# Optimization experiments

Measured on AMD Instinct MI355X. Metric: run time of the kernel, lower is better.

The kernel has to match this reference:

```python
import jax, jax.numpy as jnp
import numpy as np

N_NODES = 50000
N_EDGES = 800000
HIDDEN = 64
NUM_FEATURES = 1
OUT_DIM = 2


def setup_inputs() -> dict:
    key = jax.random.key(0)
    k = jax.random.split(key, 6)
    x = jax.random.normal(k[0], (N_NODES, NUM_FEATURES), dtype=jnp.float32)
    edge_index = jax.random.randint(k[1], (2, N_EDGES), 0, N_NODES, dtype=jnp.int32)
    # GCNConv params (PyG default: glorot weight, zero bias; random here for testing)
    W1 = jax.random.normal(k[2], (NUM_FEATURES, HIDDEN), dtype=jnp.float32) * 0.5
    b1 = jax.random.normal(k[3], (HIDDEN,), dtype=jnp.float32) * 0.1
    W2 = jax.random.normal(k[4], (HIDDEN, OUT_DIM), dtype=jnp.float32) * 0.1
    b2 = jax.random.normal(k[5], (OUT_DIM,), dtype=jnp.float32) * 0.1
    return {"x": x, "edge_index": edge_index, "W1": W1, "b1": b1, "W2": W2, "b2": b2}


def _gcn_norm(edge_index, num_nodes):
    # PyG gcn_norm with add_self_loops=True, symmetric normalization
    row, col = edge_index[0], edge_index[1]
    loop = jnp.arange(num_nodes, dtype=row.dtype)
    row = jnp.concatenate([row, loop])
    col = jnp.concatenate([col, loop])
    ew = jnp.ones(row.shape[0], dtype=jnp.float32)
    deg = jax.ops.segment_sum(ew, col, num_segments=num_nodes)  # in-degree incl. self-loop
    dinv = jnp.where(deg > 0, jax.lax.rsqrt(deg), 0.0)
    norm = dinv[row] * dinv[col]  # [E+N]
    return row, col, norm


def _gcn_conv(x, row, col, norm, W, b, num_nodes):
    h = x @ W                                  # [N, out] transform first (out <= in here is fine)
    msg = h[row] * norm[:, None]               # gather + scale, [E+N, out]
    out = jax.ops.segment_sum(msg, col, num_segments=num_nodes)  # scatter-add at targets
    return out + b


def reference(x, edge_index, W1, b1, W2, b2):
    row, col, norm = _gcn_norm(edge_index, N_NODES)
    h = _gcn_conv(x, row, col, norm, W1, b1, N_NODES)
    h = jax.nn.relu(h)
    out = _gcn_conv(h, row, col, norm, W2, b2, N_NODES)
    return out
```

## Files before the change

kernel.cpp:

```cpp
#include <hip/hip_runtime.h>
#include <math.h>

#define N_NODES 50000
#define N_EDGES 800000
#define HIDDEN  64
#define MAXDEG  64


__global__ void k_build(const int* __restrict__ row, const int* __restrict__ col,
                        int* __restrict__ cnt, unsigned short* __restrict__ ell) {
    int e = blockIdx.x * blockDim.x + threadIdx.x;
    if (e < N_EDGES) {
        int c = col[e];
        int rk = atomicAdd(&cnt[c], 1);
        if (rk < MAXDEG) ell[rk * N_NODES + c] = (unsigned short)row[e];
    }
}

__global__ void k_dinvg(const int* __restrict__ cnt, const float* __restrict__ x,
                        float* __restrict__ dinv, float* __restrict__ g) {
    int i = blockIdx.x * blockDim.x + threadIdx.x;
    if (i < N_NODES) {
        float di = rsqrtf((float)(cnt[i] + 1));
        dinv[i] = di;
        g[i] = di * x[i];
    }
}

__global__ void k_layer1(const unsigned short* __restrict__ ell,
                         const int* __restrict__ cnt, const float* __restrict__ g,
                         const float* __restrict__ dinv,
                         const float* __restrict__ W1, const float* __restrict__ b1,
                         const float* __restrict__ W2, float2* __restrict__ z) {
    int n = blockIdx.x * blockDim.x + threadIdx.x;
    if (n >= N_NODES) return;
    int d = cnt[n]; if (d > MAXDEG) d = MAXDEG;
    float acc = 0.0f;
    int j = 0;
    for (; j + 2 <= d; j += 2) {
        int r0 = ell[j * N_NODES + n];
        int r1 = ell[(j + 1) * N_NODES + n];
        acc += g[r0] + g[r1];
    }
    if (j < d) acc += g[ell[j * N_NODES + n]];
    float di = dinv[n];
    float sv = di * (acc + g[n]);
    float y0 = 0.0f, y1 = 0.0f;
#pragma unroll
    for (int k = 0; k < HIDDEN; ++k) {
        float h = fmaxf(sv * W1[k] + b1[k], 0.0f);
        y0 += h * W2[2 * k];
        y1 += h * W2[2 * k + 1];
    }
    z[n] = make_float2(di * y0, di * y1);
}

__global__ void k_layer2(const unsigned short* __restrict__ ell,
                         const int* __restrict__ cnt, const float2* __restrict__ z,
                         const float* __restrict__ dinv, const float* __restrict__ b2,
                         float* __restrict__ out) {
    int n = blockIdx.x * blockDim.x + threadIdx.x;
    if (n >= N_NODES) return;
    int d = cnt[n]; if (d > MAXDEG) d = MAXDEG;
    float T0 = 0.0f, T1 = 0.0f;
    int j = 0;
    for (; j + 2 <= d; j += 2) {
        int r0 = ell[j * N_NODES + n];
        int r1 = ell[(j + 1) * N_NODES + n];
        float2 v0 = z[r0], v1 = z[r1];
        T0 += v0.x + v1.x;
        T1 += v0.y + v1.y;
    }
    if (j < d) {
        float2 v = z[ell[j * N_NODES + n]];
        T0 += v.x; T1 += v.y;
    }
    float di = dinv[n];
    float2 zn = z[n];
    out[2 * n]     = di * (T0 + zn.x) + b2[0];
    out[2 * n + 1] = di * (T1 + zn.y) + b2[1];
}


extern "C" void kernel_launch(void* const* d_in, const int* in_sizes, int n_in,
                              void* d_out, int out_size, void* d_ws, size_t ws_size,
                              hipStream_t stream) {
    const float* x  = (const float*)d_in[0];
    const int*   ei = (const int*)d_in[1];
    const float* W1 = (const float*)d_in[2];
    const float* b1 = (const float*)d_in[3];
    const float* W2 = (const float*)d_in[4];
    const float* b2 = (const float*)d_in[5];
    float* out = (float*)d_out;

    const int* row = ei;
    const int* col = ei + N_EDGES;

    int*    ws   = (int*)d_ws;
    int*    cnt  = ws;
    float*  dinv = (float*)(ws + 1 * N_NODES);
    float*  g    = (float*)(ws + 2 * N_NODES);
    float2* z    = (float2*)(ws + 3 * N_NODES);
    unsigned short* ell = (unsigned short*)(ws + 5 * N_NODES);

    const int BE = 256, BN = 128;
    const int gE = (N_EDGES + BE - 1) / BE;
    const int gN = (N_NODES + BN - 1) / BN;

    hipMemsetAsync(cnt, 0, N_NODES * sizeof(int), stream);
    k_build<<<gE, BE, 0, stream>>>(row, col, cnt, ell);
    k_dinvg<<<gN, BN, 0, stream>>>(cnt, x, dinv, g);
    k_layer1<<<gN, BN, 0, stream>>>(ell, cnt, g, dinv, W1, b1, W2, z);
    k_layer2<<<gN, BN, 0, stream>>>(ell, cnt, z, dinv, b2, out);
}
```

Baseline: 127.8 us.

## Fuse degree-normalization into layer kernels and vectorize edge build

Removes the separate dinv/g kernel: layer1 now recomputes rsqrt(deg+1)*x for each gathered neighbor, and both layers compute their own dinv from the count. The build kernel handles two edges per thread with int2 loads, block size goes from 128 to 256 with launch bounds, and the output is written as float2. This saves one launch and the dinv/g buffers, but layer1 now does two random gathers (cnt and x) per neighbor instead of one.

Measured after the change: 128.3 us. Within noise of the previous version (+0.4%).

```diff
diff --git a/kernel.cpp b/kernel.cpp
--- a/kernel.cpp
+++ b/kernel.cpp
@@ -7,31 +7,30 @@
 #define MAXDEG  64
 
 
-__global__ void k_build(const int* __restrict__ row, const int* __restrict__ col,
-                        int* __restrict__ cnt, unsigned short* __restrict__ ell) {
-    int e = blockIdx.x * blockDim.x + threadIdx.x;
-    if (e < N_EDGES) {
+__global__ __launch_bounds__(256)
+void k_build(const int* __restrict__ row, const int* __restrict__ col,
+             int* __restrict__ cnt, unsigned short* __restrict__ ell) {
+    int i = blockIdx.x * blockDim.x + threadIdx.x;
+    int e = i * 2;
+    if (e + 1 < N_EDGES) {
+        int2 c2 = *(const int2*)(col + e);
+        int2 r2 = *(const int2*)(row + e);
+        int rk0 = atomicAdd(&cnt[c2.x], 1);
+        int rk1 = atomicAdd(&cnt[c2.y], 1);
+        if (rk0 < MAXDEG) ell[rk0 * N_NODES + c2.x] = (unsigned short)r2.x;
+        if (rk1 < MAXDEG) ell[rk1 * N_NODES + c2.y] = (unsigned short)r2.y;
+    } else if (e < N_EDGES) {
         int c = col[e];
         int rk = atomicAdd(&cnt[c], 1);
         if (rk < MAXDEG) ell[rk * N_NODES + c] = (unsigned short)row[e];
     }
 }
 
-__global__ void k_dinvg(const int* __restrict__ cnt, const float* __restrict__ x,
-                        float* __restrict__ dinv, float* __restrict__ g) {
-    int i = blockIdx.x * blockDim.x + threadIdx.x;
-    if (i < N_NODES) {
-        float di = rsqrtf((float)(cnt[i] + 1));
-        dinv[i] = di;
-        g[i] = di * x[i];
-    }
-}
-
-__global__ void k_layer1(const unsigned short* __restrict__ ell,
-                         const int* __restrict__ cnt, const float* __restrict__ g,
-                         const float* __restrict__ dinv,
-                         const float* __restrict__ W1, const float* __restrict__ b1,
-                         const float* __restrict__ W2, float2* __restrict__ z) {
+__global__ __launch_bounds__(256)
+void k_layer1(const unsigned short* __restrict__ ell, const int* __restrict__ cnt,
+              const float* __restrict__ x,
+              const float* __restrict__ W1, const float* __restrict__ b1,
+              const float* __restrict__ W2, float2* __restrict__ z) {
     int n = blockIdx.x * blockDim.x + threadIdx.x;
     if (n >= N_NODES) return;
     int d = cnt[n]; if (d > MAXDEG) d = MAXDEG;
@@ -40,11 +39,16 @@
     for (; j + 2 <= d; j += 2) {
         int r0 = ell[j * N_NODES + n];
         int r1 = ell[(j + 1) * N_NODES + n];
-        acc += g[r0] + g[r1];
+        float g0 = rsqrtf((float)(cnt[r0] + 1)) * x[r0];
+        float g1 = rsqrtf((float)(cnt[r1] + 1)) * x[r1];
+        acc += g0 + g1;
     }
-    if (j < d) acc += g[ell[j * N_NODES + n]];
-    float di = dinv[n];
-    float sv = di * (acc + g[n]);
+    if (j < d) {
+        int r = ell[j * N_NODES + n];
+        acc += rsqrtf((float)(cnt[r] + 1)) * x[r];
+    }
+    float di = rsqrtf((float)(d + 1));
+    float sv = di * (acc + di * x[n]);
     float y0 = 0.0f, y1 = 0.0f;
 #pragma unroll
     for (int k = 0; k < HIDDEN; ++k) {
@@ -55,10 +59,10 @@
     z[n] = make_float2(di * y0, di * y1);
 }
 
-__global__ void k_layer2(const unsigned short* __restrict__ ell,
-                         const int* __restrict__ cnt, const float2* __restrict__ z,
-                         const float* __restrict__ dinv, const float* __restrict__ b2,
-                         float* __restrict__ out) {
+__global__ __launch_bounds__(256)
+void k_layer2(const unsigned short* __restrict__ ell, const int* __restrict__ cnt,
+              const float2* __restrict__ z, const float* __restrict__ b2,
+              float2* __restrict__ out) {
     int n = blockIdx.x * blockDim.x + threadIdx.x;
     if (n >= N_NODES) return;
     int d = cnt[n]; if (d > MAXDEG) d = MAXDEG;
@@ -75,10 +79,9 @@
         float2 v = z[ell[j * N_NODES + n]];
         T0 += v.x; T1 += v.y;
     }
-    float di = dinv[n];
+    float di = rsqrtf((float)(d + 1));
     float2 zn = z[n];
-    out[2 * n]     = di * (T0 + zn.x) + b2[0];
-    out[2 * n + 1] = di * (T1 + zn.y) + b2[1];
+    out[n] = make_float2(di * (T0 + zn.x) + b2[0], di * (T1 + zn.y) + b2[1]);
 }
 
 
@@ -91,25 +94,20 @@
     const float* b1 = (const float*)d_in[3];
     const float* W2 = (const float*)d_in[4];
     const float* b2 = (const float*)d_in[5];
-    float* out = (float*)d_out;
 
     const int* row = ei;
     const int* col = ei + N_EDGES;
 
-    int*    ws   = (int*)d_ws;
-    int*    cnt  = ws;
-    float*  dinv = (float*)(ws + 1 * N_NODES);
-    float*  g    = (float*)(ws + 2 * N_NODES);
-    float2* z    = (float2*)(ws + 3 * N_NODES);
-    unsigned short* ell = (unsigned short*)(ws + 5 * N_NODES);
+    int*    ws  = (int*)d_ws;
+    int*    cnt = ws;
+    float2* z   = (float2*)(ws + N_NODES);
+    unsigned short* ell = (unsigned short*)(ws + 3 * N_NODES);
 
-    const int BE = 256, BN = 128;
-    const int gE = (N_EDGES + BE - 1) / BE;
-    const int gN = (N_NODES + BN - 1) / BN;
+    const int gE = (N_EDGES / 2 + 255) / 256;
+    const int gN = (N_NODES + 255) / 256;
 
     hipMemsetAsync(cnt, 0, N_NODES * sizeof(int), stream);
-    k_build<<<gE, BE, 0, stream>>>(row, col, cnt, ell);
-    k_dinvg<<<gN, BN, 0, stream>>>(cnt, x, dinv, g);
-    k_layer1<<<gN, BN, 0, stream>>>(ell, cnt, g, dinv, W1, b1, W2, z);
-    k_layer2<<<gN, BN, 0, stream>>>(ell, cnt, z, dinv, b2, out);
+    k_build <<<gE, 256, 0, stream>>>(row, col, cnt, ell);
+    k_layer1<<<gN, 256, 0, stream>>>(ell, cnt, x, W1, b1, W2, z);
+    k_layer2<<<gN, 256, 0, stream>>>(ell, cnt, z, b2, (float2*)d_out);
 }
```
